# Optimization experiments

Measured on AMD Instinct MI355X. Metric: run time of the kernel, lower is better.

## Reference

```python
import jax, jax.numpy as jnp
import numpy as np

ROUTING_ITER = 3
EPS = 1e-8


def squash(caps, axis=-1, eps=EPS):
    dot = jnp.sum(caps * caps, axis=axis, keepdims=True)
    scale = dot / (1.0 + dot) / jnp.sqrt(dot + eps)
    return scale * caps


def setup_inputs() -> dict:
    key = jax.random.key(0)
    k1, k2, k3 = jax.random.split(key, 3)
    B, I, O, D_in, D_out = 32, 1024, 64, 16, 32
    x = jax.random.normal(k1, (B, I, D_in), dtype=jnp.float32)
    W = jax.random.normal(k2, (1, I, O, D_out, D_in), dtype=jnp.float32) * 0.05
    b = jax.random.normal(k3, (1, 1, O, D_out), dtype=jnp.float32) * 0.05
    return {"x": x, "W": W, "b": b}


def reference(x, W, b):
    # u_hat[b,i,o,d] = sum_n W[0,i,o,d,n] * x[b,i,n]
    u_hat = jnp.einsum('iodn,bin->biod', W[0], x)  # [B, I, O, D_out]
    u_hat_det = jax.lax.stop_gradient(u_hat)
    B, I, O, _ = u_hat.shape
    b_ij = jnp.zeros((B, I, O, 1), dtype=x.dtype)
    v_j = None
    for it in range(ROUTING_ITER):
        c_ij = jax.nn.softmax(b_ij, axis=2)  # over output capsules
        if it == ROUTING_ITER - 1:
            s_j = jnp.sum(c_ij * u_hat, axis=1, keepdims=True) + b  # [B,1,O,D]
            v_j = squash(s_j, axis=-1)
        else:
            s_j = jnp.sum(c_ij * u_hat_det, axis=1, keepdims=True)
            v_j = squash(s_j, axis=-1)
            a_ij = jnp.sum(u_hat_det * v_j, axis=-1, keepdims=True)  # agreement
            b_ij = b_ij + a_ij
    return jnp.squeeze(v_j)  # [B, O, D_out]
```

## Files before the change

### kernel.cpp

```cpp
#include <hip/hip_runtime.h>
#include <hip/hip_bf16.h>
#include <stdint.h>

#define B_  32
#define I_  1024
#define O_  64
#define D_  32
#define N_  16
#define OD_ 2048

__device__ __forceinline__ uint32_t f2bf1(float f) {
  uint32_t u = __float_as_uint(f);
  return (u + 0x7fffu + ((u >> 16) & 1u)) >> 16;
}
__device__ __forceinline__ uint32_t pack2(float a, float b) {
  return f2bf1(a) | (f2bf1(b) << 16);
}
__device__ __forceinline__ float bflo(uint32_t v) { return __uint_as_float(v << 16); }
__device__ __forceinline__ float bfhi(uint32_t v) { return __uint_as_float(v & 0xffff0000u); }
__device__ __forceinline__ void unpack8(uint4 r, float* u) {
  u[0] = bflo(r.x); u[1] = bfhi(r.x);
  u[2] = bflo(r.y); u[3] = bfhi(r.y);
  u[4] = bflo(r.z); u[5] = bfhi(r.z);
  u[6] = bflo(r.w); u[7] = bfhi(r.w);
}

__global__ __launch_bounds__(256) void k_einsum(const float* __restrict__ x,
                                                const float* __restrict__ W,
                                                uint16_t* __restrict__ uhat) {
  const int i = blockIdx.x >> 2;
  const int q = blockIdx.x & 3;
  const int t = threadIdx.x;
  const int od0 = q * 512 + t * 2;
  __shared__ float xs[B_ * N_];
  for (int e = t; e < B_ * N_; e += 256) {
    int bb = e >> 4, n = e & 15;
    xs[e] = x[(size_t)bb * (I_ * N_) + (size_t)i * N_ + n];
  }
  float wA[16], wB[16];
  {
    const float4* Wp = (const float4*)(W + (size_t)i * (OD_ * N_) + (size_t)od0 * N_);
    #pragma unroll
    for (int qq = 0; qq < 4; ++qq) {
      float4 fa = Wp[qq];
      wA[qq * 4 + 0] = fa.x; wA[qq * 4 + 1] = fa.y;
      wA[qq * 4 + 2] = fa.z; wA[qq * 4 + 3] = fa.w;
      float4 fb = Wp[4 + qq];
      wB[qq * 4 + 0] = fb.x; wB[qq * 4 + 1] = fb.y;
      wB[qq * 4 + 2] = fb.z; wB[qq * 4 + 3] = fb.w;
    }
  }
  __syncthreads();
  uint32_t* u32 = (uint32_t*)uhat;
  #pragma unroll 2
  for (int bb = 0; bb < B_; ++bb) {
    float4 x0 = ((const float4*)(xs + bb * 16))[0];
    float4 x1 = ((const float4*)(xs + bb * 16))[1];
    float4 x2 = ((const float4*)(xs + bb * 16))[2];
    float4 x3 = ((const float4*)(xs + bb * 16))[3];
    float xv[16] = {x0.x, x0.y, x0.z, x0.w, x1.x, x1.y, x1.z, x1.w,
                    x2.x, x2.y, x2.z, x2.w, x3.x, x3.y, x3.z, x3.w};
    float a0 = 0.f, a1 = 0.f;
    #pragma unroll
    for (int n = 0; n < 16; ++n) {
      a0 = fmaf(wA[n], xv[n], a0);
      a1 = fmaf(wB[n], xv[n], a1);
    }
    u32[(((size_t)bb * I_ + i) * OD_ + od0) >> 1] = pack2(a0, a1);
  }
}

__global__ __launch_bounds__(256) void k_sum0(const uint4* __restrict__ uhat,
                                              uint4* __restrict__ part) {
  const int b = blockIdx.x >> 5, chunk = blockIdx.x & 31;
  const int t = threadIdx.x;
  float acc[8] = {0.f, 0.f, 0.f, 0.f, 0.f, 0.f, 0.f, 0.f};
  const size_t ubase = (((size_t)b * I_ + (size_t)chunk * 32) * OD_ + (size_t)t * 8) >> 3;
  #pragma unroll 8
  for (int ii = 0; ii < 32; ++ii) {
    uint4 r = uhat[ubase + (size_t)ii * (OD_ / 8)];
    float u[8]; unpack8(r, u);
    #pragma unroll
    for (int j = 0; j < 8; ++j) acc[j] += u[j];
  }
  part[(((size_t)b * 32 + chunk) * OD_ + (size_t)t * 8) >> 3] =
      make_uint4(pack2(acc[0], acc[1]), pack2(acc[2], acc[3]),
                 pack2(acc[4], acc[5]), pack2(acc[6], acc[7]));
}

__global__ __launch_bounds__(256) void k_squash(const uint16_t* __restrict__ part,
                                                const float* __restrict__ bias,
                                                float* __restrict__ vout,
                                                float scale, int addBias) {
  const int lane = threadIdx.x & 63;
  const int row = blockIdx.x * 4 + (threadIdx.x >> 6);
  const int b = row >> 6, o = row & 63;
  const int d = lane & 31;
  const uint16_t* p = part + (size_t)b * (32 * OD_) + (size_t)o * 32 + d;
  float s = 0.f;
  const int c0 = (lane >> 5) * 16;
  for (int c = c0; c < c0 + 16; ++c)
    s += __uint_as_float(((uint32_t)p[(size_t)c * OD_]) << 16);
  s += __shfl_xor(s, 32);
  s *= scale;
  if (addBias) s += bias[o * 32 + d];
  float dot = s * s;
  #pragma unroll
  for (int off = 1; off <= 16; off <<= 1) dot += __shfl_xor(dot, off);
  float sc = dot / (1.f + dot) / sqrtf(dot + 1e-8f);
  if (lane < 32) vout[(size_t)row * 32 + d] = s * sc;
}

__global__ __launch_bounds__(256) void k_route(const uint4* __restrict__ uhat,
                                               const float* __restrict__ vprev,
                                               float* __restrict__ bij,
                                               uint4* __restrict__ part,
                                               int secondIter) {
  const int b = blockIdx.x >> 5, chunk = blockIdx.x & 31;
  const int t = threadIdx.x;
  const int w = t >> 6, lane = t & 63;
  __shared__ float red[4][64][32];
  uint32_t vp[16];
  {
    const float4* vpt = (const float4*)(vprev + ((size_t)b * 64 + lane) * 32);
    #pragma unroll
    for (int q = 0; q < 8; ++q) {
      float4 f = vpt[q];
      vp[2 * q]     = pack2(f.x, f.y);
      vp[2 * q + 1] = pack2(f.z, f.w);
    }
  }
  float s_acc[32];
  #pragma unroll
  for (int d = 0; d < 32; ++d) s_acc[d] = 0.f;
  const int i0 = chunk * 32 + w * 8;
  const uint4* ub = uhat + ((size_t)b * I_ + i0) * 256 + (size_t)lane * 4;
  for (int r = 0; r < 8; ++r) {
    const uint4* uc = ub + (size_t)r * 256;
    uint4 c0 = uc[0], c1 = uc[1], c2 = uc[2], c3 = uc[3];
    float a = 0.f;
    {
      float u8[8];
      unpack8(c0, u8);
      #pragma unroll
      for (int p = 0; p < 4; ++p) {
        uint32_t vv = vp[p];
        a = fmaf(u8[2 * p], bflo(vv), a);
        a = fmaf(u8[2 * p + 1], bfhi(vv), a);
      }
      unpack8(c1, u8);
      #pragma unroll
      for (int p = 0; p < 4; ++p) {
        uint32_t vv = vp[4 + p];
        a = fmaf(u8[2 * p], bflo(vv), a);
        a = fmaf(u8[2 * p + 1], bfhi(vv), a);
      }
      unpack8(c2, u8);
      #pragma unroll
      for (int p = 0; p < 4; ++p) {
        uint32_t vv = vp[8 + p];
        a = fmaf(u8[2 * p], bflo(vv), a);
        a = fmaf(u8[2 * p + 1], bfhi(vv), a);
      }
      unpack8(c3, u8);
      #pragma unroll
      for (int p = 0; p < 4; ++p) {
        uint32_t vv = vp[12 + p];
        a = fmaf(u8[2 * p], bflo(vv), a);
        a = fmaf(u8[2 * p + 1], bfhi(vv), a);
      }
    }
    const int i = i0 + r;
    const size_t bidx = ((size_t)b * I_ + i) * 64 + lane;
    float bn = a;
    if (secondIter) bn += bij[bidx];
    else            bij[bidx] = bn;
    float m = bn;
    #pragma unroll
    for (int off = 1; off <= 32; off <<= 1) m = fmaxf(m, __shfl_xor(m, off));
    float e = __expf(bn - m);
    float sm = e;
    #pragma unroll
    for (int off = 1; off <= 32; off <<= 1) sm += __shfl_xor(sm, off);
    const float c = e / sm;
    {
      float u8[8];
      unpack8(c0, u8);
      #pragma unroll
      for (int j = 0; j < 8; ++j) s_acc[j] = fmaf(c, u8[j], s_acc[j]);
      unpack8(c1, u8);
      #pragma unroll
      for (int j = 0; j < 8; ++j) s_acc[8 + j] = fmaf(c, u8[j], s_acc[8 + j]);
      unpack8(c2, u8);
      #pragma unroll
      for (int j = 0; j < 8; ++j) s_acc[16 + j] = fmaf(c, u8[j], s_acc[16 + j]);
      unpack8(c3, u8);
      #pragma unroll
      for (int j = 0; j < 8; ++j) s_acc[24 + j] = fmaf(c, u8[j], s_acc[24 + j]);
    }
  }
  #pragma unroll
  for (int d = 0; d < 32; ++d) red[w][lane][(d + lane) & 31] = s_acc[d];
  __syncthreads();
  {
    const int o = t >> 2, db = (t & 3) * 8;
    float sum[8];
    #pragma unroll
    for (int j = 0; j < 8; ++j) {
      const int sw = (db + j + o) & 31;
      sum[j] = red[0][o][sw] + red[1][o][sw] + red[2][o][sw] + red[3][o][sw];
    }
    part[(((size_t)b * 32 + chunk) * OD_ + (size_t)t * 8) >> 3] =
        make_uint4(pack2(sum[0], sum[1]), pack2(sum[2], sum[3]),
                   pack2(sum[4], sum[5]), pack2(sum[6], sum[7]));
  }
}

extern "C" void kernel_launch(void* const* d_in, const int* in_sizes, int n_in,
                              void* d_out, int out_size, void* d_ws, size_t ws_size,
                              hipStream_t stream) {
  const float* x    = (const float*)d_in[0];
  const float* W    = (const float*)d_in[1];
  const float* bias = (const float*)d_in[2];
  float* out = (float*)d_out;

  char* ws = (char*)d_ws;
  uint16_t* uhat1 = (uint16_t*)ws;
  uint4*    uhat4 = (uint4*)ws;
  float* bij  = (float*)(ws + 134217728ull);
  uint4* part = (uint4*)(ws + 134217728ull + 8388608ull);
  uint16_t* part16 = (uint16_t*)part;
  float* vbuf = (float*)(ws + 134217728ull + 8388608ull + 4194304ull);

  k_einsum<<<dim3(I_ * 4), dim3(256), 0, stream>>>(x, W, uhat1);
  k_sum0  <<<dim3(1024), dim3(256), 0, stream>>>(uhat4, part);
  k_squash<<<dim3(512),  dim3(256), 0, stream>>>(part16, bias, vbuf, 1.f / 64.f, 0);
  k_route <<<dim3(1024), dim3(256), 0, stream>>>(uhat4, vbuf, bij, part, 0);
  k_squash<<<dim3(512),  dim3(256), 0, stream>>>(part16, bias, vbuf, 1.f, 0);
  k_route <<<dim3(1024), dim3(256), 0, stream>>>(uhat4, vbuf, bij, part, 1);
  k_squash<<<dim3(512),  dim3(256), 0, stream>>>(part16, bias, out, 1.f, 1);
}
```

Before: 298.7 us.

## Split routing into agreement and weighted-sum kernels, accumulating v instead of b_ij

```diff
diff --git a/kernel.cpp b/kernel.cpp
--- a/kernel.cpp
+++ b/kernel.cpp
@@ -88,10 +88,103 @@
                  pack2(acc[4], acc[5]), pack2(acc[6], acc[7]));
 }
 
+__global__ __launch_bounds__(256) void k_agree(const uint4* __restrict__ uhat,
+                                               const float* __restrict__ v,
+                                               float* __restrict__ cij) {
+  const int b = blockIdx.x >> 6, chunk = blockIdx.x & 63;
+  const int t = threadIdx.x;
+  const int w = t >> 6, lane = t & 63;
+  uint32_t vp[16];
+  {
+    const float4* vpt = (const float4*)(v + ((size_t)b * 64 + lane) * 32);
+    #pragma unroll
+    for (int q = 0; q < 8; ++q) {
+      float4 f = vpt[q];
+      vp[2 * q]     = pack2(f.x, f.y);
+      vp[2 * q + 1] = pack2(f.z, f.w);
+    }
+  }
+  const int i0 = chunk * 16 + w * 4;
+  const uint4* ub = uhat + ((size_t)b * I_ + i0) * 256 + (size_t)lane * 4;
+  for (int r = 0; r < 4; ++r) {
+    const uint4* uc = ub + (size_t)r * 256;
+    uint4 c0 = uc[0], c1 = uc[1], c2 = uc[2], c3 = uc[3];
+    float a = 0.f;
+    {
+      float u8[8];
+      unpack8(c0, u8);
+      #pragma unroll
+      for (int p = 0; p < 4; ++p) {
+        uint32_t vv = vp[p];
+        a = fmaf(u8[2 * p], bflo(vv), a);
+        a = fmaf(u8[2 * p + 1], bfhi(vv), a);
+      }
+      unpack8(c1, u8);
+      #pragma unroll
+      for (int p = 0; p < 4; ++p) {
+        uint32_t vv = vp[4 + p];
+        a = fmaf(u8[2 * p], bflo(vv), a);
+        a = fmaf(u8[2 * p + 1], bfhi(vv), a);
+      }
+      unpack8(c2, u8);
+      #pragma unroll
+      for (int p = 0; p < 4; ++p) {
+        uint32_t vv = vp[8 + p];
+        a = fmaf(u8[2 * p], bflo(vv), a);
+        a = fmaf(u8[2 * p + 1], bfhi(vv), a);
+      }
+      unpack8(c3, u8);
+      #pragma unroll
+      for (int p = 0; p < 4; ++p) {
+        uint32_t vv = vp[12 + p];
+        a = fmaf(u8[2 * p], bflo(vv), a);
+        a = fmaf(u8[2 * p + 1], bfhi(vv), a);
+      }
+    }
+    float m = a;
+    #pragma unroll
+    for (int off = 1; off <= 32; off <<= 1) m = fmaxf(m, __shfl_xor(m, off));
+    float e = __expf(a - m);
+    float sm = e;
+    #pragma unroll
+    for (int off = 1; off <= 32; off <<= 1) sm += __shfl_xor(sm, off);
+    cij[((size_t)b * I_ + i0 + r) * 64 + lane] = e / sm;
+  }
+}
+
+__global__ __launch_bounds__(256) void k_wsum(const uint4* __restrict__ uhat,
+                                              const float* __restrict__ cij,
+                                              uint4* __restrict__ part) {
+  const int b = blockIdx.x >> 5, chunk = blockIdx.x & 31;
+  const int t = threadIdx.x;
+  __shared__ float cs[32 * 64];
+  {
+    const float4* src = (const float4*)(cij + ((size_t)b * I_ + (size_t)chunk * 32) * 64);
+    float4* dst = (float4*)cs;
+    dst[t]       = src[t];
+    dst[t + 256] = src[t + 256];
+  }
+  __syncthreads();
+  const int o = t >> 2;
+  float acc[8] = {0.f, 0.f, 0.f, 0.f, 0.f, 0.f, 0.f, 0.f};
+  const size_t ubase = (((size_t)b * I_ + (size_t)chunk * 32) * OD_ + (size_t)t * 8) >> 3;
+  #pragma unroll 8
+  for (int ii = 0; ii < 32; ++ii) {
+    uint4 r = uhat[ubase + (size_t)ii * (OD_ / 8)];
+    const float c = cs[ii * 64 + o];
+    float u[8]; unpack8(r, u);
+    #pragma unroll
+    for (int j = 0; j < 8; ++j) acc[j] = fmaf(c, u[j], acc[j]);
+  }
+  part[(((size_t)b * 32 + chunk) * OD_ + (size_t)t * 8) >> 3] =
+      make_uint4(pack2(acc[0], acc[1]), pack2(acc[2], acc[3]),
+                 pack2(acc[4], acc[5]), pack2(acc[6], acc[7]));
+}
+
 __global__ __launch_bounds__(256) void k_squash(const uint16_t* __restrict__ part,
                                                 const float* __restrict__ bias,
                                                 float* __restrict__ vout,
-                                                float scale, int addBias) {
+                                                float scale, int addBias, int addPrev) {
   const int lane = threadIdx.x & 63;
   const int row = blockIdx.x * 4 + (threadIdx.x >> 6);
   const int b = row >> 6, o = row & 63;
@@ -108,111 +201,10 @@
   #pragma unroll
   for (int off = 1; off <= 16; off <<= 1) dot += __shfl_xor(dot, off);
   float sc = dot / (1.f + dot) / sqrtf(dot + 1e-8f);
-  if (lane < 32) vout[(size_t)row * 32 + d] = s * sc;
-}
-
-__global__ __launch_bounds__(256) void k_route(const uint4* __restrict__ uhat,
-                                               const float* __restrict__ vprev,
-                                               float* __restrict__ bij,
-                                               uint4* __restrict__ part,
-                                               int secondIter) {
-  const int b = blockIdx.x >> 5, chunk = blockIdx.x & 31;
-  const int t = threadIdx.x;
-  const int w = t >> 6, lane = t & 63;
-  __shared__ float red[4][64][32];
-  uint32_t vp[16];
-  {
-    const float4* vpt = (const float4*)(vprev + ((size_t)b * 64 + lane) * 32);
-    #pragma unroll
-    for (int q = 0; q < 8; ++q) {
-      float4 f = vpt[q];
-      vp[2 * q]     = pack2(f.x, f.y);
-      vp[2 * q + 1] = pack2(f.z, f.w);
-    }
-  }
-  float s_acc[32];
-  #pragma unroll
-  for (int d = 0; d < 32; ++d) s_acc[d] = 0.f;
-  const int i0 = chunk * 32 + w * 8;
-  const uint4* ub = uhat + ((size_t)b * I_ + i0) * 256 + (size_t)lane * 4;
-  for (int r = 0; r < 8; ++r) {
-    const uint4* uc = ub + (size_t)r * 256;
-    uint4 c0 = uc[0], c1 = uc[1], c2 = uc[2], c3 = uc[3];
-    float a = 0.f;
-    {
-      float u8[8];
-      unpack8(c0, u8);
-      #pragma unroll
-      for (int p = 0; p < 4; ++p) {
-        uint32_t vv = vp[p];
-        a = fmaf(u8[2 * p], bflo(vv), a);
-        a = fmaf(u8[2 * p + 1], bfhi(vv), a);
-      }
-      unpack8(c1, u8);
-      #pragma unroll
-      for (int p = 0; p < 4; ++p) {
-        uint32_t vv = vp[4 + p];
-        a = fmaf(u8[2 * p], bflo(vv), a);
-        a = fmaf(u8[2 * p + 1], bfhi(vv), a);
-      }
-      unpack8(c2, u8);
-      #pragma unroll
-      for (int p = 0; p < 4; ++p) {
-        uint32_t vv = vp[8 + p];
-        a = fmaf(u8[2 * p], bflo(vv), a);
-        a = fmaf(u8[2 * p + 1], bfhi(vv), a);
-      }
-      unpack8(c3, u8);
-      #pragma unroll
-      for (int p = 0; p < 4; ++p) {
-        uint32_t vv = vp[12 + p];
-        a = fmaf(u8[2 * p], bflo(vv), a);
-        a = fmaf(u8[2 * p + 1], bfhi(vv), a);
-      }
-    }
-    const int i = i0 + r;
-    const size_t bidx = ((size_t)b * I_ + i) * 64 + lane;
-    float bn = a;
-    if (secondIter) bn += bij[bidx];
-    else            bij[bidx] = bn;
-    float m = bn;
-    #pragma unroll
-    for (int off = 1; off <= 32; off <<= 1) m = fmaxf(m, __shfl_xor(m, off));
-    float e = __expf(bn - m);
-    float sm = e;
-    #pragma unroll
-    for (int off = 1; off <= 32; off <<= 1) sm += __shfl_xor(sm, off);
-    const float c = e / sm;
-    {
-      float u8[8];
-      unpack8(c0, u8);
-      #pragma unroll
-      for (int j = 0; j < 8; ++j) s_acc[j] = fmaf(c, u8[j], s_acc[j]);
-      unpack8(c1, u8);
-      #pragma unroll
-      for (int j = 0; j < 8; ++j) s_acc[8 + j] = fmaf(c, u8[j], s_acc[8 + j]);
-      unpack8(c2, u8);
-      #pragma unroll
-      for (int j = 0; j < 8; ++j) s_acc[16 + j] = fmaf(c, u8[j], s_acc[16 + j]);
-      unpack8(c3, u8);
-      #pragma unroll
-      for (int j = 0; j < 8; ++j) s_acc[24 + j] = fmaf(c, u8[j], s_acc[24 + j]);
-    }
-  }
-  #pragma unroll
-  for (int d = 0; d < 32; ++d) red[w][lane][(d + lane) & 31] = s_acc[d];
-  __syncthreads();
-  {
-    const int o = t >> 2, db = (t & 3) * 8;
-    float sum[8];
-    #pragma unroll
-    for (int j = 0; j < 8; ++j) {
-      const int sw = (db + j + o) & 31;
-      sum[j] = red[0][o][sw] + red[1][o][sw] + red[2][o][sw] + red[3][o][sw];
-    }
-    part[(((size_t)b * 32 + chunk) * OD_ + (size_t)t * 8) >> 3] =
-        make_uint4(pack2(sum[0], sum[1]), pack2(sum[2], sum[3]),
-                   pack2(sum[4], sum[5]), pack2(sum[6], sum[7]));
+  if (lane < 32) {
+    float val = s * sc;
+    if (addPrev) val += vout[(size_t)row * 32 + d];
+    vout[(size_t)row * 32 + d] = val;
   }
 }
 
@@ -227,16 +219,18 @@
   char* ws = (char*)d_ws;
   uint16_t* uhat1 = (uint16_t*)ws;
   uint4*    uhat4 = (uint4*)ws;
-  float* bij  = (float*)(ws + 134217728ull);
+  float* cij  = (float*)(ws + 134217728ull);
   uint4* part = (uint4*)(ws + 134217728ull + 8388608ull);
   uint16_t* part16 = (uint16_t*)part;
   float* vbuf = (float*)(ws + 134217728ull + 8388608ull + 4194304ull);
 
   k_einsum<<<dim3(I_ * 4), dim3(256), 0, stream>>>(x, W, uhat1);
   k_sum0  <<<dim3(1024), dim3(256), 0, stream>>>(uhat4, part);
-  k_squash<<<dim3(512),  dim3(256), 0, stream>>>(part16, bias, vbuf, 1.f / 64.f, 0);
-  k_route <<<dim3(1024), dim3(256), 0, stream>>>(uhat4, vbuf, bij, part, 0);
-  k_squash<<<dim3(512),  dim3(256), 0, stream>>>(part16, bias, vbuf, 1.f, 0);
-  k_route <<<dim3(1024), dim3(256), 0, stream>>>(uhat4, vbuf, bij, part, 1);
-  k_squash<<<dim3(512),  dim3(256), 0, stream>>>(part16, bias, out, 1.f, 1);
-}
+  k_squash<<<dim3(512),  dim3(256), 0, stream>>>(part16, bias, vbuf, 1.f / 64.f, 0, 0);
+  k_agree <<<dim3(2048), dim3(256), 0, stream>>>(uhat4, vbuf, cij);
+  k_wsum  <<<dim3(1024), dim3(256), 0, stream>>>(uhat4, cij, part);
+  k_squash<<<dim3(512),  dim3(256), 0, stream>>>(part16, bias, vbuf, 1.f, 0, 1);
+  k_agree <<<dim3(2048), dim3(256), 0, stream>>>(uhat4, vbuf, cij);
+  k_wsum  <<<dim3(1024), dim3(256), 0, stream>>>(uhat4, cij, part);
+  k_squash<<<dim3(512),  dim3(256), 0, stream>>>(part16, bias, out, 1.f, 1, 0);
+}
```

After: 336.0 us. +12.5%, slower.

## Fold routing logits into summed capsule vectors and interleave u_hat layout

Applied to the files above, without the earlier changes.

```diff
diff --git a/kernel.cpp b/kernel.cpp
--- a/kernel.cpp
+++ b/kernel.cpp
@@ -8,6 +8,7 @@
 #define D_  32
 #define N_  16
 #define OD_ 2048
+
 
 __device__ __forceinline__ uint32_t f2bf1(float f) {
   uint32_t u = __float_as_uint(f);
@@ -31,7 +32,10 @@
   const int i = blockIdx.x >> 2;
   const int q = blockIdx.x & 3;
   const int t = threadIdx.x;
-  const int od0 = q * 512 + t * 2;
+  const int u = q * 256 + t;
+  const int o  = (u >> 2) & 63;
+  const int dp = u & 3;
+  const int od0 = o * 32 + q * 8 + dp * 2;
   __shared__ float xs[B_ * N_];
   for (int e = t; e < B_ * N_; e += 256) {
     int bb = e >> 4, n = e & 15;
@@ -66,7 +70,7 @@
       a0 = fmaf(wA[n], xv[n], a0);
       a1 = fmaf(wB[n], xv[n], a1);
     }
-    u32[(((size_t)bb * I_ + i) * OD_ + od0) >> 1] = pack2(a0, a1);
+    u32[((size_t)bb * I_ + i) * 1024 + u] = pack2(a0, a1);
   }
 }
 
@@ -91,12 +95,13 @@
 __global__ __launch_bounds__(256) void k_squash(const uint16_t* __restrict__ part,
                                                 const float* __restrict__ bias,
                                                 float* __restrict__ vout,
-                                                float scale, int addBias) {
+                                                float scale, int addBias, int addPrev) {
   const int lane = threadIdx.x & 63;
   const int row = blockIdx.x * 4 + (threadIdx.x >> 6);
   const int b = row >> 6, o = row & 63;
   const int d = lane & 31;
-  const uint16_t* p = part + (size_t)b * (32 * OD_) + (size_t)o * 32 + d;
+  const uint16_t* p = part + (size_t)b * (32 * OD_) +
+                      (size_t)(d >> 3) * 512 + (size_t)o * 8 + (d & 7);
   float s = 0.f;
   const int c0 = (lane >> 5) * 16;
   for (int c = c0; c < c0 + 16; ++c)
@@ -108,14 +113,16 @@
   #pragma unroll
   for (int off = 1; off <= 16; off <<= 1) dot += __shfl_xor(dot, off);
   float sc = dot / (1.f + dot) / sqrtf(dot + 1e-8f);
-  if (lane < 32) vout[(size_t)row * 32 + d] = s * sc;
+  if (lane < 32) {
+    float val = s * sc;
+    if (addPrev) val += vout[(size_t)row * 32 + d];
+    vout[(size_t)row * 32 + d] = val;
+  }
 }
 
 __global__ __launch_bounds__(256) void k_route(const uint4* __restrict__ uhat,
                                                const float* __restrict__ vprev,
-                                               float* __restrict__ bij,
-                                               uint4* __restrict__ part,
-                                               int secondIter) {
+                                               uint4* __restrict__ part) {
   const int b = blockIdx.x >> 5, chunk = blockIdx.x & 31;
   const int t = threadIdx.x;
   const int w = t >> 6, lane = t & 63;
@@ -134,10 +141,10 @@
   #pragma unroll
   for (int d = 0; d < 32; ++d) s_acc[d] = 0.f;
   const int i0 = chunk * 32 + w * 8;
-  const uint4* ub = uhat + ((size_t)b * I_ + i0) * 256 + (size_t)lane * 4;
+  const uint4* ub = uhat + ((size_t)b * I_ + i0) * 256 + lane;
   for (int r = 0; r < 8; ++r) {
     const uint4* uc = ub + (size_t)r * 256;
-    uint4 c0 = uc[0], c1 = uc[1], c2 = uc[2], c3 = uc[3];
+    uint4 c0 = uc[0], c1 = uc[64], c2 = uc[128], c3 = uc[192];
     float a = 0.f;
     {
       float u8[8];
@@ -170,15 +177,10 @@
         a = fmaf(u8[2 * p + 1], bfhi(vv), a);
       }
     }
-    const int i = i0 + r;
-    const size_t bidx = ((size_t)b * I_ + i) * 64 + lane;
-    float bn = a;
-    if (secondIter) bn += bij[bidx];
-    else            bij[bidx] = bn;
-    float m = bn;
+    float m = a;
     #pragma unroll
     for (int off = 1; off <= 32; off <<= 1) m = fmaxf(m, __shfl_xor(m, off));
-    float e = __expf(bn - m);
+    float e = __expf(a - m);
     float sm = e;
     #pragma unroll
     for (int off = 1; off <= 32; off <<= 1) sm += __shfl_xor(sm, off);
@@ -203,14 +205,14 @@
   for (int d = 0; d < 32; ++d) red[w][lane][(d + lane) & 31] = s_acc[d];
   __syncthreads();
   {
-    const int o = t >> 2, db = (t & 3) * 8;
+    const int o = t & 63, k = t >> 6;
     float sum[8];
     #pragma unroll
     for (int j = 0; j < 8; ++j) {
-      const int sw = (db + j + o) & 31;
+      const int sw = (k * 8 + j + o) & 31;
       sum[j] = red[0][o][sw] + red[1][o][sw] + red[2][o][sw] + red[3][o][sw];
     }
-    part[(((size_t)b * 32 + chunk) * OD_ + (size_t)t * 8) >> 3] =
+    part[((size_t)b * 32 + chunk) * 256 + t] =
         make_uint4(pack2(sum[0], sum[1]), pack2(sum[2], sum[3]),
                    pack2(sum[4], sum[5]), pack2(sum[6], sum[7]));
   }
@@ -227,16 +229,15 @@
   char* ws = (char*)d_ws;
   uint16_t* uhat1 = (uint16_t*)ws;
   uint4*    uhat4 = (uint4*)ws;
-  float* bij  = (float*)(ws + 134217728ull);
   uint4* part = (uint4*)(ws + 134217728ull + 8388608ull);
   uint16_t* part16 = (uint16_t*)part;
   float* vbuf = (float*)(ws + 134217728ull + 8388608ull + 4194304ull);
 
   k_einsum<<<dim3(I_ * 4), dim3(256), 0, stream>>>(x, W, uhat1);
   k_sum0  <<<dim3(1024), dim3(256), 0, stream>>>(uhat4, part);
-  k_squash<<<dim3(512),  dim3(256), 0, stream>>>(part16, bias, vbuf, 1.f / 64.f, 0);
-  k_route <<<dim3(1024), dim3(256), 0, stream>>>(uhat4, vbuf, bij, part, 0);
-  k_squash<<<dim3(512),  dim3(256), 0, stream>>>(part16, bias, vbuf, 1.f, 0);
-  k_route <<<dim3(1024), dim3(256), 0, stream>>>(uhat4, vbuf, bij, part, 1);
-  k_squash<<<dim3(512),  dim3(256), 0, stream>>>(part16, bias, out, 1.f, 1);
-}
+  k_squash<<<dim3(512),  dim3(256), 0, stream>>>(part16, bias, vbuf, 1.f / 64.f, 0, 0);
+  k_route <<<dim3(1024), dim3(256), 0, stream>>>(uhat4, vbuf, part);
+  k_squash<<<dim3(512),  dim3(256), 0, stream>>>(part16, bias, vbuf, 1.f, 0, 1);
+  k_route <<<dim3(1024), dim3(256), 0, stream>>>(uhat4, vbuf, part);
+  k_squash<<<dim3(512),  dim3(256), 0, stream>>>(part16, bias, out, 1.f, 1, 0);
+}
```

Measured after the change: 295.6 us. About the same (-1.0%).
